# Kernel tuning notes

Measured on AMD Instinct MI355X. Metric: run time of the kernel, lower is better.

Reference implementation:

```python
import jax, jax.numpy as jnp
import numpy as np

FEAT_STRIDE = 8
IM_DIMS = (4096.0, 4096.0)  # (height, width)
ANCHOR_SCALES = (8.0, 16.0, 32.0)
RATIOS = (0.5, 1.0, 2.0)
PRE_NMS_TOPN = 12000   # TRAIN cfg (eval_mode=False)
POST_NMS_TOPN = 2000
NMS_THRESH = 0.7
MIN_SIZE = 16.0


def _generate_anchors(base_size=16.0, ratios=RATIOS, scales=ANCHOR_SCALES):
    ratios = np.array(ratios, np.float32)
    scales = np.array(scales, np.float32)
    w = h = float(base_size)
    x_ctr = 0.5 * (w - 1.0)
    y_ctr = 0.5 * (h - 1.0)
    size = w * h
    ws = np.round(np.sqrt(size / ratios))
    hs = np.round(ws * ratios)
    out = []
    for wr, hr in zip(ws, hs):
        wss = wr * scales
        hss = hr * scales
        out.append(np.stack([x_ctr - 0.5 * (wss - 1.0), y_ctr - 0.5 * (hss - 1.0),
                             x_ctr + 0.5 * (wss - 1.0), y_ctr + 0.5 * (hss - 1.0)], axis=1))
    return np.concatenate(out, 0).astype(np.float32)  # [A=9, 4]


def _nms(boxes, scores, thresh, max_out):
    # greedy sequential NMS; indices are discrete -> stop gradients here
    boxes = jax.lax.stop_gradient(boxes)
    scores = jax.lax.stop_gradient(scores)
    areas = (boxes[:, 2] - boxes[:, 0] + 1.0) * (boxes[:, 3] - boxes[:, 1] + 1.0)

    def body(i, state):
        supp, keep = state
        idx = jnp.argmax(jnp.where(supp, -jnp.inf, scores))
        b = boxes[idx]
        xx1 = jnp.maximum(b[0], boxes[:, 0])
        yy1 = jnp.maximum(b[1], boxes[:, 1])
        xx2 = jnp.minimum(b[2], boxes[:, 2])
        yy2 = jnp.minimum(b[3], boxes[:, 3])
        inter = jnp.maximum(0.0, xx2 - xx1 + 1.0) * jnp.maximum(0.0, yy2 - yy1 + 1.0)
        iou = inter / (areas[idx] + areas - inter)
        supp = supp | (iou > thresh)  # also suppresses idx itself (iou==1)
        keep = keep.at[i].set(idx.astype(jnp.int32))
        return supp, keep

    supp0 = jnp.zeros(boxes.shape[0], dtype=bool)
    keep0 = jnp.zeros(max_out, dtype=jnp.int32)
    _, keep = jax.lax.fori_loop(0, max_out, body, (supp0, keep0))
    return keep


def reference(rpn_cls_score, rpn_bbox_pred):
    _, H, W, C2 = rpn_cls_score.shape
    A = C2 // 2
    # rpn_softmax: per-anchor 2-way (bg, fg) softmax; channels laid out [2, A]
    prob = jax.nn.softmax(rpn_cls_score.reshape(H, W, 2, A), axis=2)
    scores = prob[:, :, 1, :].reshape(-1)           # fg scores, [H*W*A]
    deltas = rpn_bbox_pred.reshape(-1, 4)           # [H*W*A, 4]

    # anchors shifted over the feature grid
    anchors = jnp.asarray(_generate_anchors())       # [A, 4]
    sx = jnp.arange(W, dtype=jnp.float32) * FEAT_STRIDE
    sy = jnp.arange(H, dtype=jnp.float32) * FEAT_STRIDE
    shift_x, shift_y = jnp.meshgrid(sx, sy)          # [H, W]
    shifts = jnp.stack([shift_x, shift_y, shift_x, shift_y], -1).reshape(-1, 1, 4)
    all_anchors = (anchors[None, :, :] + shifts).reshape(-1, 4)  # [H*W*A, 4]

    # bbox_transform_inv
    ws = all_anchors[:, 2] - all_anchors[:, 0] + 1.0
    hs = all_anchors[:, 3] - all_anchors[:, 1] + 1.0
    cx = all_anchors[:, 0] + 0.5 * ws
    cy = all_anchors[:, 1] + 0.5 * hs
    dx, dy, dw, dh = deltas[:, 0], deltas[:, 1], deltas[:, 2], deltas[:, 3]
    pcx = dx * ws + cx
    pcy = dy * hs + cy
    pw = jnp.exp(dw) * ws
    ph = jnp.exp(dh) * hs
    x1 = pcx - 0.5 * pw
    y1 = pcy - 0.5 * ph
    x2 = pcx + 0.5 * pw
    y2 = pcy + 0.5 * ph

    # clip to image boundaries
    x1 = jnp.clip(x1, 0.0, IM_DIMS[1] - 1.0)
    y1 = jnp.clip(y1, 0.0, IM_DIMS[0] - 1.0)
    x2 = jnp.clip(x2, 0.0, IM_DIMS[1] - 1.0)
    y2 = jnp.clip(y2, 0.0, IM_DIMS[0] - 1.0)
    proposals = jnp.stack([x1, y1, x2, y2], axis=1)

    # drop tiny boxes (jit-friendly: -inf score instead of physical removal)
    keep_min = ((x2 - x1 + 1.0) >= MIN_SIZE) & ((y2 - y1 + 1.0) >= MIN_SIZE)
    scores = jnp.where(keep_min, scores, -jnp.inf)

    top_scores, order = jax.lax.top_k(scores, PRE_NMS_TOPN)
    props = proposals[order]                         # [pre_nms_topN, 4]
    keep = _nms(props, top_scores, NMS_THRESH, POST_NMS_TOPN)
    rois = props[keep]                               # [post_nms_topN, 4]
    # blob: [batch_idx(=0), x1, y1, x2, y2]
    return jnp.concatenate([jnp.zeros((POST_NMS_TOPN, 1), rois.dtype), rois], axis=1)


def setup_inputs() -> dict:
    key = jax.random.key(0)
    k1, k2 = jax.random.split(key)
    rpn_cls_score = jax.random.normal(k1, (1, 512, 512, 18), dtype=jnp.float32)
    rpn_bbox_pred = jax.random.normal(k2, (1, 512, 512, 36), dtype=jnp.float32) * 0.2
    return {"rpn_cls_score": rpn_cls_score, "rpn_bbox_pred": rpn_bbox_pred}
```

## Files before the change

kernel.cpp:

```cpp
#include <hip/hip_runtime.h>
#include <cstdint>
#include <cstddef>

#pragma clang fp contract(off)

#define N_ANCH 2359296
#define K_PRE  12000
#define K_POST 2000
#define NWORD  188
#define NC     94
#define TIE_CAP 65536

typedef unsigned int u32;
typedef unsigned long long u64;

__constant__ float c_anch[9][4] = {
  { -84.f,  -40.f,   99.f,   55.f },
  { -176.f, -88.f,  191.f,  103.f },
  { -360.f, -184.f, 375.f,  199.f },
  { -56.f,  -56.f,   71.f,   71.f },
  { -120.f, -120.f, 135.f,  135.f },
  { -248.f, -248.f, 263.f,  263.f },
  { -36.f,  -80.f,   51.f,   95.f },
  { -80.f,  -168.f,  95.f,  183.f },
  { -168.f, -344.f, 183.f,  359.f },
};

__device__ __forceinline__ float pexpf(float xin) {
#pragma clang fp contract(off)
  const float exp_hi = 88.3762626647950f;
  const float exp_lo = -88.3762626647949f;
  const float LOG2EF = 1.44269504088896341f;
  const float C1 = 0.693359375f;
  const float C2 = -2.12194440e-4f;
  const float p0 = 1.9875691500E-4f;
  const float p1 = 1.3981999507E-3f;
  const float p2 = 8.3334519073E-3f;
  const float p3 = 4.1665795894E-2f;
  const float p4 = 1.6666665459E-1f;
  const float p5 = 5.0000001201E-1f;
  float x = fminf(fmaxf(xin, exp_lo), exp_hi);
  float fx = floorf(x * LOG2EF + 0.5f);
  float tmp = C1 * fx;
  float z = C2 * fx;
  x = x - tmp;
  x = x - z;
  z = x * x;
  float y = x * p0 + p1;
  y = y * x + p2;
  y = y * x + p3;
  y = y * x + p4;
  y = y * x + p5;
  y = y * z + x;
  y = 1.0f + y;
  int n = (int)fx;
  u32 e = ((u32)(n + 127)) << 23;
  return y * __uint_as_float(e);
}

__device__ __forceinline__ void decode_box(const float* __restrict__ bbox, int aidx,
                                           float4* ob, float* oarea, bool* okeep) {
#pragma clang fp contract(off)
  int pos = aidx / 9;
  int a = aidx - pos * 9;
  int w = pos & 511;
  int h = pos >> 9;
  float shx = (float)(w * 8);
  float shy = (float)(h * 8);
  float ax1 = c_anch[a][0] + shx;
  float ay1 = c_anch[a][1] + shy;
  float ax2 = c_anch[a][2] + shx;
  float ay2 = c_anch[a][3] + shy;
  float aw = (ax2 - ax1) + 1.0f;
  float ah = (ay2 - ay1) + 1.0f;
  float acx = ax1 + 0.5f * aw;
  float acy = ay1 + 0.5f * ah;
  const float* d = bbox + (size_t)pos * 36 + (size_t)a * 4;
  float dx = d[0], dy = d[1], dw = d[2], dh = d[3];
  float pcx = dx * aw + acx;
  float pcy = dy * ah + acy;
  float pw = pexpf(dw) * aw;
  float ph = pexpf(dh) * ah;
  float x1 = pcx - 0.5f * pw;
  float y1 = pcy - 0.5f * ph;
  float x2 = pcx + 0.5f * pw;
  float y2 = pcy + 0.5f * ph;
  x1 = fminf(fmaxf(x1, 0.0f), 4095.0f);
  y1 = fminf(fmaxf(y1, 0.0f), 4095.0f);
  x2 = fminf(fmaxf(x2, 0.0f), 4095.0f);
  y2 = fminf(fmaxf(y2, 0.0f), 4095.0f);
  *ob = make_float4(x1, y1, x2, y2);
  float ww = (x2 - x1) + 1.0f;
  float hh = (y2 - y1) + 1.0f;
  *oarea = ww * hh;
  *okeep = (ww >= 16.0f) && (hh >= 16.0f);
}

__global__ void k_scores(const float* __restrict__ cls, const float* __restrict__ bbox,
                         u32* __restrict__ keys, u32* __restrict__ ctl,
                         u32* __restrict__ hist) {
#pragma clang fp contract(off)
  int t = blockIdx.x * blockDim.x + threadIdx.x;
  if (blockIdx.x == 0) {
    if (threadIdx.x < 16) ctl[threadIdx.x] = (threadIdx.x == 1) ? (u32)K_PRE : 0u;
    hist[threadIdx.x] = 0u;
  }
  if (t >= N_ANCH) return;
  int pos = t / 9;
  int a = t - pos * 9;
  float s0 = cls[(size_t)pos * 18 + a];
  float s1 = cls[(size_t)pos * 18 + 9 + a];
  float m = fmaxf(s0, s1);
  float e0 = pexpf(s0 - m);
  float e1 = pexpf(s1 - m);
  float p = e1 / (e0 + e1);
  float4 box; float area; bool km;
  decode_box(bbox, t, &box, &area, &km);
  keys[t] = km ? (__float_as_uint(p) | 0x80000000u) : 0u;
}

__global__ void k_histscan(const u32* __restrict__ keys, u32* __restrict__ ctl,
                           u32* __restrict__ hist, int shift, int pass) {
  __shared__ u32 lh[4][256];
  __shared__ u32 s_last;
  int t = threadIdx.x;
  lh[0][t] = 0u; lh[1][t] = 0u; lh[2][t] = 0u; lh[3][t] = 0u;
  __syncthreads();
  int sub = t & 3;
  u32 prefix = ctl[0];
  u32 msk = (shift == 24) ? 0u : (0xFFFFFFFFu << (shift + 8));
  int stride = gridDim.x * blockDim.x;
  for (int i = blockIdx.x * blockDim.x + t; i < N_ANCH; i += stride) {
    u32 k = keys[i];
    if ((k & msk) == prefix) atomicAdd(&lh[sub][(k >> shift) & 0xFFu], 1u);
  }
  __syncthreads();
  u32 hsum = lh[0][t] + lh[1][t] + lh[2][t] + lh[3][t];
  if (hsum) atomicAdd(&hist[t], hsum);
  __syncthreads();
  if (t == 0) {
    __threadfence();
    u32 old = atomicAdd(&ctl[8 + pass], 1u);
    s_last = (old == gridDim.x - 1) ? 1u : 0u;
  }
  __syncthreads();
  if (!s_last) return;
  __threadfence();
  __shared__ u32 sh[256];
  __shared__ u32 horig[256];
  __shared__ int s_d;
  u32 h = atomicAdd(&hist[t], 0u);
  sh[t] = h; horig[t] = h;
  if (t == 0) s_d = 0;
  u32 krem = ctl[1];
  __syncthreads();
  u32 v = h;
  for (int off = 1; off < 256; off <<= 1) {
    u32 add = (t + off < 256) ? sh[t + off] : 0u;
    __syncthreads();
    v += add;
    sh[t] = v;
    __syncthreads();
  }
  if (sh[t] >= krem) atomicMax(&s_d, t);
  __syncthreads();
  if (t == 0) {
    int d = s_d;
    u32 cum = sh[d] - horig[d];
    ctl[0] |= ((u32)d) << shift;
    ctl[1] = krem - cum;
    if (shift == 0) { ctl[2] = ctl[0]; ctl[3] = ctl[1]; }
  }
  hist[t] = 0u;
}

__global__ void k_collect(const u32* __restrict__ keys, u32* __restrict__ ctl,
                          int* __restrict__ sel, int* __restrict__ tie,
                          u64* __restrict__ comps) {
  __shared__ int stI[2048];
  __shared__ u64 stC[2048];
  __shared__ int stT[256];
  __shared__ u32 s_cnt, s_tcnt, s_base, s_tbase;
  int tid = threadIdx.x;
  if (tid == 0) { s_cnt = 0; s_tcnt = 0; }
  __syncthreads();
  u32 kstar = ctl[2];
  int stride = gridDim.x * blockDim.x;
  for (int i = blockIdx.x * blockDim.x + tid; i < N_ANCH; i += stride) {
    u32 k = keys[i];
    if (k > kstar) {
      u32 p = atomicAdd(&s_cnt, 1u);
      u64 cmp = ((u64)k << 32) | (u64)(0xFFFFFFFFu - (u32)i);
      if (p < 2048u) { stI[p] = i; stC[p] = cmp; }
      else { u32 g = atomicAdd(&ctl[4], 1u); sel[g] = i; comps[g] = cmp; }
    } else if (k == kstar) {
      u32 p = atomicAdd(&s_tcnt, 1u);
      if (p < 256u) stT[p] = i;
      else { u32 g = atomicAdd(&ctl[5], 1u); if (g < TIE_CAP) tie[g] = i; }
    }
  }
  __syncthreads();
  if (tid == 0) {
    u32 n = min(s_cnt, 2048u);
    s_base = atomicAdd(&ctl[4], n);
    u32 tn = min(s_tcnt, 256u);
    s_tbase = atomicAdd(&ctl[5], tn);
  }
  __syncthreads();
  u32 n = min(s_cnt, 2048u);
  for (u32 q = tid; q < n; q += blockDim.x) {
    sel[s_base + q] = stI[q];
    comps[s_base + q] = stC[q];
  }
  u32 tn = min(s_tcnt, 256u);
  for (u32 q = tid; q < tn; q += blockDim.x) {
    u32 g = s_tbase + q;
    if (g < TIE_CAP) tie[g] = stT[q];
  }
}

__global__ void k_tiepick(const u32* __restrict__ ctl, const int* __restrict__ tie,
                          int* __restrict__ sel, u64* __restrict__ comps) {
  u32 T = ctl[5]; if (T > TIE_CAP) T = TIE_CAP;
  if (T > 8192u) T = 8192u;
  u32 need = ctl[3];
  u32 base = ctl[4];
  u32 kstar = ctl[2];
  for (u32 t = threadIdx.x; t < T; t += blockDim.x) {
    int v = tie[t];
    u32 r = 0;
    for (u32 u = 0; u < T; ++u) r += (tie[u] < v) ? 1u : 0u;
    if (r < need) {
      sel[base + r] = v;
      comps[base + r] = ((u64)kstar << 32) | (u64)(0xFFFFFFFFu - (u32)v);
    }
  }
}

__global__ void k_rankdec(const u64* __restrict__ comps, const int* __restrict__ sel,
                          const float* __restrict__ bbox,
                          float4* __restrict__ props, float* __restrict__ areas) {
  int lane = threadIdx.x & 63;
  int wave = threadIdx.x >> 6;
  int base = (blockIdx.x * 4 + wave) * 8;
  u64 c0 = comps[base + 0], c1 = comps[base + 1], c2 = comps[base + 2], c3 = comps[base + 3];
  u64 c4 = comps[base + 4], c5 = comps[base + 5], c6 = comps[base + 6], c7 = comps[base + 7];
  int n0 = 0, n1 = 0, n2 = 0, n3 = 0, n4 = 0, n5 = 0, n6 = 0, n7 = 0;
#pragma unroll 4
  for (int j = lane; j < K_PRE; j += 64) {
    u64 v = comps[j];
    n0 += (v > c0); n1 += (v > c1); n2 += (v > c2); n3 += (v > c3);
    n4 += (v > c4); n5 += (v > c5); n6 += (v > c6); n7 += (v > c7);
  }
  for (int off = 32; off; off >>= 1) {
    n0 += __shfl_xor(n0, off); n1 += __shfl_xor(n1, off);
    n2 += __shfl_xor(n2, off); n3 += __shfl_xor(n3, off);
    n4 += __shfl_xor(n4, off); n5 += __shfl_xor(n5, off);
    n6 += __shfl_xor(n6, off); n7 += __shfl_xor(n7, off);
  }
  int rk = n0;
  rk = (lane == 1) ? n1 : rk; rk = (lane == 2) ? n2 : rk;
  rk = (lane == 3) ? n3 : rk; rk = (lane == 4) ? n4 : rk;
  rk = (lane == 5) ? n5 : rk; rk = (lane == 6) ? n6 : rk;
  rk = (lane == 7) ? n7 : rk;
  if (lane < 8) {
    float4 box; float area; bool km;
    decode_box(bbox, sel[base + lane], &box, &area, &km);
    props[rk] = box;
    areas[rk] = area;
  }
}

__device__ __forceinline__ int d2idx(int c, int h, int lane) {
  return ((c * 2 + h) * 64 + lane) * 2;
}

__global__ void k_mask(const float4* __restrict__ props, const float* __restrict__ areas,
                       u64* __restrict__ mask, u64* __restrict__ diag2,
                       u64* __restrict__ sub2) {
#pragma clang fp contract(off)
  int x = blockIdx.x, y = blockIdx.y;
  int cx = x >> 1, cy = y >> 1;
  if (cy + 1 < cx || cy == cx + 1) return;
  __shared__ float4 bj[64];
  __shared__ float aj[64];
  int j0 = y * 64;
  bj[threadIdx.x] = props[j0 + threadIdx.x];
  aj[threadIdx.x] = areas[j0 + threadIdx.x];
  __syncthreads();
  int i = x * 64 + threadIdx.x;
  float4 bi = props[i];
  float ai = areas[i];
  u64 bits = 0;
  for (int jj = 0; jj < 64; ++jj) {
    int j = j0 + jj;
    float4 bb = bj[jj];
    float xx1 = fmaxf(bi.x, bb.x);
    float yy1 = fmaxf(bi.y, bb.y);
    float xx2 = fminf(bi.z, bb.z);
    float yy2 = fminf(bi.w, bb.w);
    float w = fmaxf(0.0f, (xx2 - xx1) + 1.0f);
    float h = fmaxf(0.0f, (yy2 - yy1) + 1.0f);
    float inter = w * h;
    float iou = inter / ((ai + aj[jj]) - inter);
    if ((iou > 0.7f) && (j < K_PRE)) bits |= (1ull << jj);
  }
  if (cy == cx)          diag2[d2idx(cx, x & 1, threadIdx.x) + (y & 1)] = bits;
  else if (cy == cx - 1) sub2[d2idx(cx, x & 1, threadIdx.x) + (y & 1)] = bits;
  else                   mask[(size_t)i * NWORD + y] = bits;
}

#define NMS_BAR() asm volatile("s_waitcnt lgkmcnt(0)\n\ts_barrier" ::: "memory")

typedef __attribute__((address_space(1))) const u32* gas_p;
typedef __attribute__((address_space(3))) u32* las_p;
__device__ __forceinline__ void gll16(const u64* g, u64* l) {
  __builtin_amdgcn_global_load_lds((gas_p)g, (las_p)l, 16, 0, 0);
}

__global__ void __launch_bounds__(1024) k_nms(const u64* __restrict__ mask,
                                              const u64* __restrict__ diag2,
                                              const u64* __restrict__ sub2,
                                              const float4* __restrict__ props,
                                              float* __restrict__ out) {
  __shared__ u64 rem[NWORD];
  __shared__ int keepb[K_POST];
  __shared__ int kept[2][128];
  __shared__ u64 dstage[2][2][64][2];
  __shared__ u64 sstage[2][2][64][2];
  __shared__ int s_kk[2];
  __shared__ int s_nk;
  __shared__ int s_brk;
  int tid = threadIdx.x;
  int lane = tid & 63;
  int wave = tid >> 6;
  for (int w = tid; w < NWORD; w += 1024) {
    int base = w * 64;
    u64 v;
    if (base + 64 <= K_PRE) v = 0ull;
    else if (base >= K_PRE) v = ~0ull;
    else v = (~0ull) << (K_PRE - base);
    rem[w] = v;
  }
  if (tid == 0) { s_nk = 0; s_brk = 0; s_kk[0] = 0; s_kk[1] = 0; }
  if (wave == 0) {
    gll16(diag2 + d2idx(0, 0, lane), &dstage[0][0][0][0]);
    gll16(diag2 + d2idx(0, 1, lane), &dstage[0][1][0][0]);
    gll16(sub2 + d2idx(1, 0, lane), &sstage[1][0][0][0]);
    gll16(sub2 + d2idx(1, 1, lane), &sstage[1][1][0][0]);
  }
  __syncthreads();

  int nk = 0;

  for (int c = 0; c < NC; ++c) {
    if (s_brk) break;
    int par = c & 1;
    if (wave == 0) {
      int cn = min(c + 1, NC - 1);
      int cs = min(c + 2, NC - 1);
      gll16(diag2 + d2idx(cn, 0, lane), &dstage[cn & 1][0][0][0]);
      gll16(diag2 + d2idx(cn, 1, lane), &dstage[cn & 1][1][0][0]);
      gll16(sub2 + d2idx(cs, 0, lane), &sstage[cs & 1][0][0][0]);
      gll16(sub2 + d2idx(cs, 1, lane), &sstage[cs & 1][1][0][0]);
      asm volatile("s_waitcnt vmcnt(4)" ::: "memory");
      u64 dl0A = dstage[par][0][lane][0], dl1A = dstage[par][0][lane][1];
      u64 dh0A = dstage[par][1][lane][0], dh1A = dstage[par][1][lane][1];
      int ps = (c + 1) & 1;
      u64 sl0A = sstage[ps][0][lane][0], sl1A = sstage[ps][0][lane][1];
      u64 sh0A = sstage[ps][1][lane][0], sh1A = sstage[ps][1][lane][1];
      u64 w0 = ~rem[2 * c];
      u64 w1 = ~rem[2 * c + 1];
      u64 km0 = 0, km1 = 0;
      int nk0 = nk;
      while (w0 != 0ull && nk < K_POST) {
        int j = (int)__builtin_ctzll(w0);
        u64 sup = __ballot((int)((dl0A >> j) & 1ull));
        km0 |= (1ull << j);
        nk++;
        w0 &= ~sup;
      }
      if (km0) w1 &= ~__ballot((int)((dh0A & km0) != 0ull));
      while (w1 != 0ull && nk < K_POST) {
        int j = (int)__builtin_ctzll(w1);
        u64 sup = __ballot((int)((dh1A >> j) & 1ull));
        km1 |= (1ull << j);
        nk++;
        w1 &= ~sup;
      }
      int ncnt0 = __popcll(km0);
      u64 below = (1ull << lane) - 1ull;
      if ((km0 >> lane) & 1ull) {
        int pos = nk0 + __popcll(km0 & below);
        int idx = (c << 7) | lane;
        keepb[pos] = idx;
        kept[par][pos - nk0] = idx;
      }
      if ((km1 >> lane) & 1ull) {
        int pos = nk0 + ncnt0 + __popcll(km1 & below);
        int idx = (c << 7) | 64 | lane;
        keepb[pos] = idx;
        kept[par][pos - nk0] = idx;
      }
      if (c + 1 < NC) {
        int plo = (int)((((sl0A & km0) | (sl1A & km1)) != 0ull) ? 1 : 0);
        int phi = (int)((((sh0A & km0) | (sh1A & km1)) != 0ull) ? 1 : 0);
        u64 vlo = __ballot(plo);
        u64 vhi = __ballot(phi);
        if (lane == 0) {
          if (vlo) atomicOr((unsigned long long*)&rem[2 * c + 2], (unsigned long long)vlo);
          if (vhi) atomicOr((unsigned long long*)&rem[2 * c + 3], (unsigned long long)vhi);
        }
      }
      if (lane == 0) { s_kk[par] = nk - nk0; s_nk = nk; s_brk = (nk >= K_POST) ? 1 : 0; }
    } else if (c >= 1) {
      int kkp = s_kk[par ^ 1];
      const int* kb = &kept[par ^ 1][0];
      int wv = wave - 1;
      int seg = wv % 3;
      int q0 = wv / 3;
      int w = 2 * c + 2 + seg * 64 + lane;
      if (kkp > q0 && w < NWORD) {
        u64 fp0 = 0, fp1 = 0, fp2 = 0, fp3 = 0, fp4 = 0, fp5 = 0, fp6 = 0, fp7 = 0;
        fp0 = mask[(size_t)kb[q0] * NWORD + w];
        if (q0 + 5  < kkp) fp1 = mask[(size_t)kb[q0 + 5]  * NWORD + w];
        if (q0 + 10 < kkp) fp2 = mask[(size_t)kb[q0 + 10] * NWORD + w];
        if (q0 + 15 < kkp) fp3 = mask[(size_t)kb[q0 + 15] * NWORD + w];
        if (q0 + 20 < kkp) fp4 = mask[(size_t)kb[q0 + 20] * NWORD + w];
        if (q0 + 25 < kkp) fp5 = mask[(size_t)kb[q0 + 25] * NWORD + w];
        if (q0 + 30 < kkp) fp6 = mask[(size_t)kb[q0 + 30] * NWORD + w];
        if (q0 + 35 < kkp) fp7 = mask[(size_t)kb[q0 + 35] * NWORD + w];
        u64 v = (fp0 | fp1) | (fp2 | fp3) | ((fp4 | fp5) | (fp6 | fp7));
        for (int q = q0 + 40; q < kkp; q += 5)
          v |= mask[(size_t)kb[q] * NWORD + w];
        if (v) atomicOr((unsigned long long*)&rem[w], (unsigned long long)v);
      }
    }
    NMS_BAR();
  }
  __syncthreads();
  int fnk = s_nk;
  for (int t = tid; t < K_POST; t += 1024) {
    int kidx = (t < fnk) ? keepb[t] : 0;
    float4 b = props[kidx];
    out[t * 5 + 0] = 0.0f;
    out[t * 5 + 1] = b.x;
    out[t * 5 + 2] = b.y;
    out[t * 5 + 3] = b.z;
    out[t * 5 + 4] = b.w;
  }
}

extern "C" void kernel_launch(void* const* d_in, const int* in_sizes, int n_in,
                              void* d_out, int out_size, void* d_ws, size_t ws_size,
                              hipStream_t stream) {
  const float* cls  = (const float*)d_in[0];
  const float* bbox = (const float*)d_in[1];
  float* out = (float*)d_out;
  char* ws = (char*)d_ws;

  u64* mask    = (u64*)ws;
  u32* keys    = (u32*)ws;
  u32* ctl     = (u32*)(ws + 9437184);
  u32* hist    = (u32*)(ws + 9437248);
  int* sel     = (int*)(ws + 9438464);
  int* tie     = (int*)(ws + 9486592);
  u64* comps   = (u64*)(ws + 18096128);
  float4* props= (float4*)(ws + 18240512);
  float* areas = (float*)(ws + 18433024);
  u64* diag2   = (u64*)(ws + 18481152);
  u64* sub2    = (u64*)(ws + 18673664);

  k_scores<<<dim3((N_ANCH + 255) / 256), dim3(256), 0, stream>>>(cls, bbox, keys, ctl, hist);
  const int shifts[4] = {24, 16, 8, 0};
  for (int s = 0; s < 4; ++s)
    k_histscan<<<dim3(256), dim3(256), 0, stream>>>(keys, ctl, hist, shifts[s], s);
  k_collect<<<dim3(256), dim3(256), 0, stream>>>(keys, ctl, sel, tie, comps);
  k_tiepick<<<dim3(1), dim3(256), 0, stream>>>(ctl, tie, sel, comps);
  k_rankdec<<<dim3(375), dim3(256), 0, stream>>>(comps, sel, bbox, props, areas);
  k_mask<<<dim3(188, 188), dim3(64), 0, stream>>>(props, areas, mask, diag2, sub2);
  k_nms<<<dim3(1), dim3(1024), 0, stream>>>(mask, diag2, sub2, props, out);
}
```

Before: 317.6 us.

## Deepen NMS pipeline with second sub-diagonal mask stage and prefetched mask loads

New measurement: 347.5 us. +9.4%, slower.

```diff
diff --git a/kernel.cpp b/kernel.cpp
--- a/kernel.cpp
+++ b/kernel.cpp
@@ -277,11 +277,12 @@
 
 __global__ void k_mask(const float4* __restrict__ props, const float* __restrict__ areas,
                        u64* __restrict__ mask, u64* __restrict__ diag2,
-                       u64* __restrict__ sub2) {
+                       u64* __restrict__ sub2, u64* __restrict__ sub4) {
 #pragma clang fp contract(off)
   int x = blockIdx.x, y = blockIdx.y;
   int cx = x >> 1, cy = y >> 1;
-  if (cy + 1 < cx || cy == cx + 1) return;
+  bool wd = (cy == cx), ws2 = (cy == cx - 1), ws4 = (cy == cx - 2), wf = (cy >= cx + 3);
+  if (!(wd || ws2 || ws4 || wf)) return;
   __shared__ float4 bj[64];
   __shared__ float aj[64];
   int j0 = y * 64;
@@ -305,9 +306,10 @@
     float iou = inter / ((ai + aj[jj]) - inter);
     if ((iou > 0.7f) && (j < K_PRE)) bits |= (1ull << jj);
   }
-  if (cy == cx)          diag2[d2idx(cx, x & 1, threadIdx.x) + (y & 1)] = bits;
-  else if (cy == cx - 1) sub2[d2idx(cx, x & 1, threadIdx.x) + (y & 1)] = bits;
-  else                   mask[(size_t)i * NWORD + y] = bits;
+  if (wd)       __builtin_nontemporal_store(bits, &diag2[d2idx(cx, x & 1, threadIdx.x) + (y & 1)]);
+  else if (ws2) __builtin_nontemporal_store(bits, &sub2[d2idx(cx, x & 1, threadIdx.x) + (y & 1)]);
+  else if (ws4) __builtin_nontemporal_store(bits, &sub4[d2idx(cx, x & 1, threadIdx.x) + (y & 1)]);
+  else          __builtin_nontemporal_store(bits, &mask[(size_t)i * NWORD + y]);
 }
 
 #define NMS_BAR() asm volatile("s_waitcnt lgkmcnt(0)\n\ts_barrier" ::: "memory")
@@ -321,14 +323,17 @@
 __global__ void __launch_bounds__(1024) k_nms(const u64* __restrict__ mask,
                                               const u64* __restrict__ diag2,
                                               const u64* __restrict__ sub2,
+                                              const u64* __restrict__ sub4,
                                               const float4* __restrict__ props,
                                               float* __restrict__ out) {
   __shared__ u64 rem[NWORD];
   __shared__ int keepb[K_POST];
-  __shared__ int kept[2][128];
+  __shared__ int kept[4][128];
+  __shared__ int s_kk[4];
+  __shared__ u64 s_km0[2], s_km1[2];
   __shared__ u64 dstage[2][2][64][2];
   __shared__ u64 sstage[2][2][64][2];
-  __shared__ int s_kk[2];
+  __shared__ u64 s4stage[2][2][64][2];
   __shared__ int s_nk;
   __shared__ int s_brk;
   int tid = threadIdx.x;
@@ -342,7 +347,9 @@
     else v = (~0ull) << (K_PRE - base);
     rem[w] = v;
   }
-  if (tid == 0) { s_nk = 0; s_brk = 0; s_kk[0] = 0; s_kk[1] = 0; }
+  if (tid == 0) { s_nk = 0; s_brk = 0; }
+  if (tid < 4) s_kk[tid] = 0;
+  if (tid < 2) { s_km0[tid] = 0; s_km1[tid] = 0; }
   if (wave == 0) {
     gll16(diag2 + d2idx(0, 0, lane), &dstage[0][0][0][0]);
     gll16(diag2 + d2idx(0, 1, lane), &dstage[0][1][0][0]);
@@ -351,6 +358,8 @@
   }
   __syncthreads();
 
+  u64 fa0 = 0, fa1 = 0, fa2 = 0, fa3 = 0, fa4 = 0, fa5 = 0, fa6 = 0, fa7 = 0;
+  u64 fb0 = 0, fb1 = 0, fb2 = 0, fb3 = 0, fb4 = 0, fb5 = 0, fb6 = 0, fb7 = 0;
   int nk = 0;
 
   for (int c = 0; c < NC; ++c) {
@@ -363,12 +372,17 @@
       gll16(diag2 + d2idx(cn, 1, lane), &dstage[cn & 1][1][0][0]);
       gll16(sub2 + d2idx(cs, 0, lane), &sstage[cs & 1][0][0][0]);
       gll16(sub2 + d2idx(cs, 1, lane), &sstage[cs & 1][1][0][0]);
-      asm volatile("s_waitcnt vmcnt(4)" ::: "memory");
+      gll16(sub4 + d2idx(cs, 0, lane), &s4stage[cs & 1][0][0][0]);
+      gll16(sub4 + d2idx(cs, 1, lane), &s4stage[cs & 1][1][0][0]);
+      asm volatile("s_waitcnt vmcnt(6)" ::: "memory");
       u64 dl0A = dstage[par][0][lane][0], dl1A = dstage[par][0][lane][1];
       u64 dh0A = dstage[par][1][lane][0], dh1A = dstage[par][1][lane][1];
       int ps = (c + 1) & 1;
       u64 sl0A = sstage[ps][0][lane][0], sl1A = sstage[ps][0][lane][1];
       u64 sh0A = sstage[ps][1][lane][0], sh1A = sstage[ps][1][lane][1];
+      u64 s4l0 = s4stage[ps][0][lane][0], s4l1 = s4stage[ps][0][lane][1];
+      u64 s4h0 = s4stage[ps][1][lane][0], s4h1 = s4stage[ps][1][lane][1];
+      u64 km0p = s_km0[par ^ 1], km1p = s_km1[par ^ 1];
       u64 w0 = ~rem[2 * c];
       u64 w1 = ~rem[2 * c + 1];
       u64 km0 = 0, km1 = 0;
@@ -394,46 +408,75 @@
         int pos = nk0 + __popcll(km0 & below);
         int idx = (c << 7) | lane;
         keepb[pos] = idx;
-        kept[par][pos - nk0] = idx;
+        kept[c & 3][pos - nk0] = idx;
       }
       if ((km1 >> lane) & 1ull) {
         int pos = nk0 + ncnt0 + __popcll(km1 & below);
         int idx = (c << 7) | 64 | lane;
         keepb[pos] = idx;
-        kept[par][pos - nk0] = idx;
+        kept[c & 3][pos - nk0] = idx;
       }
       if (c + 1 < NC) {
         int plo = (int)((((sl0A & km0) | (sl1A & km1)) != 0ull) ? 1 : 0);
         int phi = (int)((((sh0A & km0) | (sh1A & km1)) != 0ull) ? 1 : 0);
         u64 vlo = __ballot(plo);
         u64 vhi = __ballot(phi);
+        if (c >= 1 && (km0p | km1p)) {
+          vlo |= __ballot((int)((((s4l0 & km0p) | (s4l1 & km1p)) != 0ull) ? 1 : 0));
+          vhi |= __ballot((int)((((s4h0 & km0p) | (s4h1 & km1p)) != 0ull) ? 1 : 0));
+        }
         if (lane == 0) {
           if (vlo) atomicOr((unsigned long long*)&rem[2 * c + 2], (unsigned long long)vlo);
           if (vhi) atomicOr((unsigned long long*)&rem[2 * c + 3], (unsigned long long)vhi);
         }
       }
-      if (lane == 0) { s_kk[par] = nk - nk0; s_nk = nk; s_brk = (nk >= K_POST) ? 1 : 0; }
-    } else if (c >= 1) {
-      int kkp = s_kk[par ^ 1];
-      const int* kb = &kept[par ^ 1][0];
+      if (lane == 0) {
+        s_kk[c & 3] = nk - nk0;
+        s_km0[par] = km0; s_km1[par] = km1;
+        s_nk = nk;
+        s_brk = (nk >= K_POST) ? 1 : 0;
+      }
+    } else {
+      __builtin_amdgcn_sched_barrier(0);
       int wv = wave - 1;
       int seg = wv % 3;
       int q0 = wv / 3;
-      int w = 2 * c + 2 + seg * 64 + lane;
-      if (kkp > q0 && w < NWORD) {
-        u64 fp0 = 0, fp1 = 0, fp2 = 0, fp3 = 0, fp4 = 0, fp5 = 0, fp6 = 0, fp7 = 0;
-        fp0 = mask[(size_t)kb[q0] * NWORD + w];
-        if (q0 + 5  < kkp) fp1 = mask[(size_t)kb[q0 + 5]  * NWORD + w];
-        if (q0 + 10 < kkp) fp2 = mask[(size_t)kb[q0 + 10] * NWORD + w];
-        if (q0 + 15 < kkp) fp3 = mask[(size_t)kb[q0 + 15] * NWORD + w];
-        if (q0 + 20 < kkp) fp4 = mask[(size_t)kb[q0 + 20] * NWORD + w];
-        if (q0 + 25 < kkp) fp5 = mask[(size_t)kb[q0 + 25] * NWORD + w];
-        if (q0 + 30 < kkp) fp6 = mask[(size_t)kb[q0 + 30] * NWORD + w];
-        if (q0 + 35 < kkp) fp7 = mask[(size_t)kb[q0 + 35] * NWORD + w];
-        u64 v = (fp0 | fp1) | (fp2 | fp3) | ((fp4 | fp5) | (fp6 | fp7));
-        for (int q = q0 + 40; q < kkp; q += 5)
-          v |= mask[(size_t)kb[q] * NWORD + w];
-        if (v) atomicOr((unsigned long long*)&rem[w], (unsigned long long)v);
+      if (c >= 2) {
+        int kkC = s_kk[(c - 2) & 3];
+        int wP = 2 * c + 2 + seg * 64 + lane;
+        if (kkC > q0 && wP < NWORD) {
+          u64 v = (par == 0) ? (fb0 | fb1 | fb2 | fb3 | fb4 | fb5 | fb6 | fb7)
+                             : (fa0 | fa1 | fa2 | fa3 | fa4 | fa5 | fa6 | fa7);
+          const int* kbC = &kept[(c - 2) & 3][0];
+          for (int q = q0 + 40; q < kkC; q += 5)
+            v |= mask[(size_t)kbC[q] * NWORD + wP];
+          if (v) atomicOr((unsigned long long*)&rem[wP], (unsigned long long)v);
+        }
+      }
+      {
+        int kkI = (c >= 1) ? s_kk[(c - 1) & 3] : 0;
+        const int* kbI = &kept[(c - 1) & 3][0];
+        int wI = 2 * c + 4 + seg * 64 + lane;
+        bool act = (c >= 1) && (kkI > q0) && (wI < NWORD);
+        if (par == 0) {
+          fa0 = act ? mask[(size_t)kbI[q0] * NWORD + wI] : 0ull;
+          fa1 = (act && q0 + 5  < kkI) ? mask[(size_t)kbI[q0 + 5]  * NWORD + wI] : 0ull;
+          fa2 = (act && q0 + 10 < kkI) ? mask[(size_t)kbI[q0 + 10] * NWORD + wI] : 0ull;
+          fa3 = (act && q0 + 15 < kkI) ? mask[(size_t)kbI[q0 + 15] * NWORD + wI] : 0ull;
+          fa4 = (act && q0 + 20 < kkI) ? mask[(size_t)kbI[q0 + 20] * NWORD + wI] : 0ull;
+          fa5 = (act && q0 + 25 < kkI) ? mask[(size_t)kbI[q0 + 25] * NWORD + wI] : 0ull;
+          fa6 = (act && q0 + 30 < kkI) ? mask[(size_t)kbI[q0 + 30] * NWORD + wI] : 0ull;
+          fa7 = (act && q0 + 35 < kkI) ? mask[(size_t)kbI[q0 + 35] * NWORD + wI] : 0ull;
+        } else {
+          fb0 = act ? mask[(size_t)kbI[q0] * NWORD + wI] : 0ull;
+          fb1 = (act && q0 + 5  < kkI) ? mask[(size_t)kbI[q0 + 5]  * NWORD + wI] : 0ull;
+          fb2 = (act && q0 + 10 < kkI) ? mask[(size_t)kbI[q0 + 10] * NWORD + wI] : 0ull;
+          fb3 = (act && q0 + 15 < kkI) ? mask[(size_t)kbI[q0 + 15] * NWORD + wI] : 0ull;
+          fb4 = (act && q0 + 20 < kkI) ? mask[(size_t)kbI[q0 + 20] * NWORD + wI] : 0ull;
+          fb5 = (act && q0 + 25 < kkI) ? mask[(size_t)kbI[q0 + 25] * NWORD + wI] : 0ull;
+          fb6 = (act && q0 + 30 < kkI) ? mask[(size_t)kbI[q0 + 30] * NWORD + wI] : 0ull;
+          fb7 = (act && q0 + 35 < kkI) ? mask[(size_t)kbI[q0 + 35] * NWORD + wI] : 0ull;
+        }
       }
     }
     NMS_BAR();
@@ -470,6 +513,7 @@
   float* areas = (float*)(ws + 18433024);
   u64* diag2   = (u64*)(ws + 18481152);
   u64* sub2    = (u64*)(ws + 18673664);
+  u64* sub4    = (u64*)(ws + 18866176);
 
   k_scores<<<dim3((N_ANCH + 255) / 256), dim3(256), 0, stream>>>(cls, bbox, keys, ctl, hist);
   const int shifts[4] = {24, 16, 8, 0};
@@ -478,6 +522,6 @@
   k_collect<<<dim3(256), dim3(256), 0, stream>>>(keys, ctl, sel, tie, comps);
   k_tiepick<<<dim3(1), dim3(256), 0, stream>>>(ctl, tie, sel, comps);
   k_rankdec<<<dim3(375), dim3(256), 0, stream>>>(comps, sel, bbox, props, areas);
-  k_mask<<<dim3(188, 188), dim3(64), 0, stream>>>(props, areas, mask, diag2, sub2);
-  k_nms<<<dim3(1), dim3(1024), 0, stream>>>(mask, diag2, sub2, props, out);
-}
+  k_mask<<<dim3(188, 188), dim3(64), 0, stream>>>(props, areas, mask, diag2, sub2, sub4);
+  k_nms<<<dim3(1), dim3(1024), 0, stream>>>(mask, diag2, sub2, sub4, props, out);
+}
```
